# Optimization experiments

Measured on AMD Instinct MI355X. Metric: run time of the kernel, lower is better.

Reference implementation:

```python
import jax, jax.numpy as jnp
import numpy as np

D, H, G, HD = 2048, 16, 4, 128  # d_model, num_heads, num_groups, head_dim
B, S = 2, 2048


def _rope(x):
    # x: [B, heads, S, HD]; RoPE with concat(freqs, freqs) layout (rotate_half style)
    seq = x.shape[2]
    inv_freq = 1.0 / (10000.0 ** (jnp.arange(0, HD, 2, dtype=jnp.float32) / HD))  # [HD/2]
    t = jnp.arange(seq, dtype=jnp.float32)
    freqs = t[:, None] * inv_freq[None, :]              # [S, HD/2]
    emb = jnp.concatenate([freqs, freqs], axis=-1)      # [S, HD]
    cos = jnp.cos(emb)[None, None]                      # [1,1,S,HD]
    sin = jnp.sin(emb)[None, None]
    x1, x2 = jnp.split(x, 2, axis=-1)
    rot = jnp.concatenate([-x2, x1], axis=-1)           # rotate_half
    return x * cos + rot * sin


def setup_inputs() -> dict:
    key = jax.random.key(0)
    ks = jax.random.split(key, 5)
    x = jax.random.normal(ks[0], (B, S, D), dtype=jnp.float32)
    # weights stored as [in, out] so y = x @ W (equivalent to torch Linear with W^T)
    Wq = jax.random.normal(ks[1], (D, D), dtype=jnp.float32) * 0.02
    Wk = jax.random.normal(ks[2], (D, G * HD), dtype=jnp.float32) * 0.02
    Wv = jax.random.normal(ks[3], (D, G * HD), dtype=jnp.float32) * 0.02
    Wo = jax.random.normal(ks[4], (D, D), dtype=jnp.float32) * 0.02
    # causal mask: True = masked (matches torch masked_fill semantics)
    mask = ~jnp.tril(jnp.ones((S, S), dtype=bool))[None, None]  # [1,1,S,S]
    return {"x": x, "Wq": Wq, "Wk": Wk, "Wv": Wv, "Wo": Wo, "mask": mask}


def reference(x, Wq, Wk, Wv, Wo, mask):
    b, s, _ = x.shape
    q = (x @ Wq).reshape(b, s, H, HD).transpose(0, 2, 1, 3)   # [B,H,S,HD]
    k = (x @ Wk).reshape(b, s, G, HD).transpose(0, 2, 1, 3)   # [B,G,S,HD]
    v = (x @ Wv).reshape(b, s, G, HD).transpose(0, 2, 1, 3)   # [B,G,S,HD]
    q = _rope(q)
    k = _rope(k)
    # GQA: repeat_interleave KV groups across heads
    k = jnp.repeat(k, H // G, axis=1)                         # [B,H,S,HD]
    v = jnp.repeat(v, H // G, axis=1)
    scale = jnp.float32(1.0 / np.sqrt(HD))
    scores = jnp.einsum('bhqd,bhkd->bhqk', q, k) * scale      # [B,H,S,S]
    scores = jnp.where(mask, jnp.float32(-1e9), scores)
    attn = jax.nn.softmax(scores, axis=-1)
    ctx = jnp.einsum('bhqk,bhkd->bhqd', attn, v)              # [B,H,S,HD]
    ctx = ctx.transpose(0, 2, 1, 3).reshape(b, s, D)
    return ctx @ Wo
```

## Files before the change

### kernel.cpp

```cpp
#include <hip/hip_runtime.h>
#include <hip/hip_bf16.h>
#include <math.h>

#define BB 2
#define SS 2048
#define DD 2048
#define HH 16
#define GG 4
#define HDIM 128
#define DKV (GG * HDIM)
#define MS (BB * SS)
#define QKVS 3072

typedef __attribute__((ext_vector_type(8))) short bf16x8;
typedef __attribute__((ext_vector_type(4))) float f32x4;
typedef __attribute__((ext_vector_type(4))) unsigned int u32x4;

__device__ __forceinline__ ushort f2bf(float x) {
    __hip_bfloat16 b = __float2bfloat16(x);
    return *(ushort*)&b;
}
__device__ __forceinline__ float bf2f(ushort u) {
    __hip_bfloat16 b;
    *(ushort*)&b = u;
    return __bfloat162float(b);
}

#define GLOAD_LDS(src, dst)                                                        \
    __builtin_amdgcn_global_load_lds(                                              \
        (const __attribute__((address_space(1))) unsigned int*)(src),              \
        (__attribute__((address_space(3))) unsigned int*)(dst), 16, 0, 0)

#define WAITV(n) asm volatile("s_waitcnt vmcnt(" #n ")" ::: "memory")

__global__ void cast_bf16(const float* __restrict__ X, ushort* __restrict__ O, int total8) {
    int idx = blockIdx.x * blockDim.x + threadIdx.x;
    if (idx >= total8) return;
    const float4* p = (const float4*)X + (size_t)idx * 2;
    float4 a = p[0], b = p[1];
    float v[8] = {a.x, a.y, a.z, a.w, b.x, b.y, b.z, b.w};
    ushort r[8];
#pragma unroll
    for (int j = 0; j < 8; ++j) r[j] = f2bf(v[j]);
    *((u32x4*)O + idx) = *(u32x4*)r;
}

__global__ __launch_bounds__(256) void transpose_cast3(const float* __restrict__ Wq,
                                                       const float* __restrict__ Wk,
                                                       const float* __restrict__ Wv,
                                                       ushort* __restrict__ WqkvT) {
    __shared__ ushort tile[32][33];
    const int z = blockIdx.z;
    if (z > 0 && blockIdx.x >= DKV / 32) return;
    const float* W = (z == 0) ? Wq : (z == 1) ? Wk : Wv;
    ushort* WT = WqkvT + ((z == 0) ? (size_t)0 : (z == 1) ? (size_t)DD * DD
                                                          : (size_t)(DD + DKV) * DD);
    const int N = (z == 0) ? DD : DKV;
    const int tx = threadIdx.x & 31, ty = threadIdx.x >> 5;
    const int n0 = blockIdx.x * 32, k0 = blockIdx.y * 32;
#pragma unroll
    for (int i = 0; i < 4; ++i)
        tile[ty + i * 8][tx] = f2bf(W[(size_t)(k0 + ty + i * 8) * N + n0 + tx]);
    __syncthreads();
#pragma unroll
    for (int i = 0; i < 4; ++i)
        WT[(size_t)(n0 + ty + i * 8) * DD + k0 + tx] = tile[tx][ty + i * 8];
}

__global__ __launch_bounds__(256) void transpose_cast(const float* __restrict__ W,
                                                      ushort* __restrict__ WT,
                                                      int K, int N) {
    __shared__ ushort tile[32][33];
    const int tx = threadIdx.x & 31, ty = threadIdx.x >> 5;
    const int n0 = blockIdx.x * 32, k0 = blockIdx.y * 32;
#pragma unroll
    for (int i = 0; i < 4; ++i)
        tile[ty + i * 8][tx] = f2bf(W[(size_t)(k0 + ty + i * 8) * N + n0 + tx]);
    __syncthreads();
#pragma unroll
    for (int i = 0; i < 4; ++i)
        WT[(size_t)(n0 + ty + i * 8) * K + k0 + tx] = tile[tx][ty + i * 8];
}

__global__ __launch_bounds__(256) void transpose_v(const ushort* __restrict__ QKV,
                                                   ushort* __restrict__ VT) {
    __shared__ ushort tile[32][33];
    const int tx = threadIdx.x & 31, ty = threadIdx.x >> 5;
    const int d0 = blockIdx.x * 32;
    const int k0 = blockIdx.y * 32;
    const int b = blockIdx.z;
#pragma unroll
    for (int i = 0; i < 4; ++i)
        tile[ty + i * 8][tx] =
            QKV[(size_t)(b * SS + k0 + ty + i * 8) * QKVS + 2560 + d0 + tx];
    __syncthreads();
    const int posl = ((tx & 12) << 1) | ((tx & 16) >> 2) | (tx & 3);
#pragma unroll
    for (int i = 0; i < 4; ++i)
        VT[((size_t)b * DKV + d0 + ty + i * 8) * SS + k0 + posl] = tile[tx][ty + i * 8];
}

template <int BN, bool OUT_BF16>
__global__ __launch_bounds__(512) void gemm8(const ushort* __restrict__ A,
                                             const ushort* __restrict__ BT,
                                             void* __restrict__ Cout,
                                             int M, int N, int K) {
    constexpr int ABUF = 128 * 32;
    constexpr int BBUF = BN * 32;
    constexpr int NWC = BN / 64;
    constexpr int NWM = 8 / NWC;
    constexpr int ROWS = 128 / NWM;
    constexpr int MFR = ROWS / 16;
    __shared__ ushort As[3 * ABUF];
    __shared__ ushort Bs[3 * BBUF];

    const int t = threadIdx.x;
    const int w = t >> 6, l = t & 63;
    const int lm = l & 15, lw = l >> 4;
    const int wr = w / NWC, wc = w % NWC;
    const int nx = gridDim.x;
    const int bid = blockIdx.y * nx + blockIdx.x;
    const int cpx = (nx * gridDim.y) >> 3;
    const int swb = (bid & 7) * cpx + (bid >> 3);
    const int bm = (swb / nx) * 128, bn = (swb % nx) * BN;

    const int NT = K >> 5;
    const int swzc = (lw ^ ((lm >> 1) & 3)) * 8;

    const int ar0 = t >> 2, ac0 = (t & 3) ^ ((ar0 >> 1) & 3);
    const ushort* a0 = A + (size_t)(bm + ar0) * K + ac0 * 8;
    const int br0 = t >> 2, bc0 = (t & 3) ^ ((br0 >> 1) & 3);
    const ushort* b0 = BT + (size_t)(bn + br0) * K + bc0 * 8;
    const int br1 = (t + 512) >> 2, bc1 = ((t + 512) & 3) ^ ((br1 >> 1) & 3);
    const ushort* b1 = BT + (size_t)(bn + br1) * K + bc1 * 8;

    auto STAGE = [&](int slot) {
        GLOAD_LDS(a0, &As[slot * ABUF + t * 8]);
        a0 += 32;
        GLOAD_LDS(b0, &Bs[slot * BBUF + t * 8]);
        b0 += 32;
        if constexpr (BN == 256) {
            GLOAD_LDS(b1, &Bs[slot * BBUF + (t + 512) * 8]);
            b1 += 32;
        }
    };

    f32x4 acc[MFR][4];
#pragma unroll
    for (int m = 0; m < MFR; ++m)
#pragma unroll
        for (int n = 0; n < 4; ++n) acc[m][n] = (f32x4){0.f, 0.f, 0.f, 0.f};

    STAGE(0);
    STAGE(1);
    int cs = 0, ps = 2;

#pragma unroll 1
    for (int kt = 0; kt < NT; ++kt) {
        if (kt + 1 < NT) {
            if constexpr (BN == 256) WAITV(3); else WAITV(2);
        } else {
            WAITV(0);
        }
        __builtin_amdgcn_s_barrier();
        if (kt + 2 < NT) STAGE(ps);

        const ushort* Ab = &As[cs * ABUF];
        const ushort* Bb = &Bs[cs * BBUF];
        bf16x8 bfr[4], af[MFR];
#pragma unroll
        for (int n = 0; n < 4; ++n)
            bfr[n] = *(const bf16x8*)&Bb[(wc * 64 + n * 16 + lm) * 32 + swzc];
#pragma unroll
        for (int i = 0; i < MFR; ++i)
            af[i] = *(const bf16x8*)&Ab[(wr * ROWS + i * 16 + lm) * 32 + swzc];
        __builtin_amdgcn_s_setprio(1);
#pragma unroll
        for (int i = 0; i < MFR; ++i)
#pragma unroll
            for (int n = 0; n < 4; ++n)
                acc[i][n] = __builtin_amdgcn_mfma_f32_16x16x32_bf16(af[i], bfr[n], acc[i][n], 0, 0, 0);
        __builtin_amdgcn_s_setprio(0);

        cs = (cs == 2) ? 0 : cs + 1;
        ps = (ps == 2) ? 0 : ps + 1;
    }

#pragma unroll
    for (int m = 0; m < MFR; ++m)
#pragma unroll
        for (int n = 0; n < 4; ++n)
#pragma unroll
            for (int r = 0; r < 4; ++r) {
                int row = bm + wr * ROWS + m * 16 + lw * 4 + r;
                int col = bn + wc * 64 + n * 16 + lm;
                if (OUT_BF16)
                    ((ushort*)Cout)[(size_t)row * N + col] = f2bf(acc[m][n][r]);
                else
                    ((float*)Cout)[(size_t)row * N + col] = acc[m][n][r];
            }
}

__global__ void rope_bf16(ushort* __restrict__ X, int total) {
    int idx = blockIdx.x * blockDim.x + threadIdx.x;
    if (idx >= total) return;
    int i = idx & 63;
    int hh = (idx >> 6) % 20;
    int row = idx / (64 * 20);
    int s = row & (SS - 1);
    int colOff = (hh < 16) ? hh * HDIM : 2048 + (hh - 16) * HDIM;
    float inv = exp2f((float)i * -0.2076205059304601f);
    float ang = (float)s * inv;
    float c, sn;
    __sincosf(ang, &sn, &c);
    size_t base = (size_t)row * QKVS + colOff + i;
    float x1 = bf2f(X[base]), x2 = bf2f(X[base + 64]);
    X[base] = f2bf(x1 * c - x2 * sn);
    X[base + 64] = f2bf(x2 * c + x1 * sn);
}

#define SCL 0.08838834764831845f
#define CEXP 0.1275296340545927f
#define THRRAW 90.50966799187809f

__global__ __launch_bounds__(512) void attn_mfma(const ushort* __restrict__ QKV,
                                                 const ushort* __restrict__ VT,
                                                 ushort* __restrict__ Ctx) {
    __shared__ ushort Ks[3][64 * 128];
    __shared__ ushort Vs[3][128 * 64];
    const int t = threadIdx.x;
    const int w = t >> 6;
    const int l = t & 63;
    const int lm = l & 15, lw = l >> 4;
    const int bid = blockIdx.x;
    const int g = bid & 3;
    const int b = (bid >> 2) & 1;
    const int within = bid >> 3;
    const int xq = within & 7;
    const int h = g * 4 + (within >> 3);
    const int swz = (lm & 7) << 3;

    const ushort* kbase = QKV + (size_t)(b * SS) * QKVS + 2048 + g * HDIM;
    const ushort* vbase = VT + ((size_t)b * DKV + g * HDIM) * SS;

    const short one_bf = (short)0x3F80;
    const bf16x8 ones = {one_bf, one_bf, one_bf, one_bf, one_bf, one_bf, one_bf, one_bf};

    const int kr0 = t >> 4, ko0 = t & 15;
    const int kr1 = (t + 512) >> 4, ko1 = (t + 512) & 15;
    const int vr0 = t >> 3, vo0 = t & 7;
    const int vr1 = (t + 512) >> 3, vo1 = (t + 512) & 7;

#pragma unroll 1
    for (int phase = 0; phase < 2; ++phase) {
        const int qt = (phase == 0) ? xq : (15 - xq);
        const int q0 = qt * 128;
        const int qw = q0 + w * 16;
        const int q = qw + lm;
        const int ntiles = 2 * qt + 2;
        const int lt = (qw + 15) >> 6;

        const ushort* ks0 = kbase + (size_t)kr0 * QKVS + ((ko0 ^ (kr0 & 7)) * 8);
        const ushort* ks1 = kbase + (size_t)kr1 * QKVS + ((ko1 ^ (kr1 & 7)) * 8);
        const ushort* vs0 = vbase + (size_t)vr0 * SS + ((vo0 ^ (vr0 & 7)) * 8);
        const ushort* vs1 = vbase + (size_t)vr1 * SS + ((vo1 ^ (vr1 & 7)) * 8);

        auto STAGE = [&](int slot) {
            GLOAD_LDS(ks0, &Ks[slot][t * 8]);
            ks0 += 64 * QKVS;
            GLOAD_LDS(ks1, &Ks[slot][(t + 512) * 8]);
            ks1 += 64 * QKVS;
            GLOAD_LDS(vs0, &Vs[slot][t * 8]);
            vs0 += 64;
            GLOAD_LDS(vs1, &Vs[slot][(t + 512) * 8]);
            vs1 += 64;
        };

        bf16x8 qa[4];
        {
            const ushort* qp = QKV + (size_t)(b * SS + qw + lm) * QKVS + h * HDIM + lw * 8;
#pragma unroll
            for (int kk = 0; kk < 4; ++kk)
                qa[kk] = *(const bf16x8*)(qp + kk * 32);
        }

        f32x4 acc[8];
#pragma unroll
        for (int d = 0; d < 8; ++d) acc[d] = (f32x4){0.f, 0.f, 0.f, 0.f};
        f32x4 accl = (f32x4){0.f, 0.f, 0.f, 0.f};
        float m = -INFINITY;

        STAGE(0);
        STAGE(1);
        int cs = 0, ps = 2;

#pragma unroll 1
        for (int tile = 0; tile < ntiles; ++tile) {
            const int kv0 = tile * 64;
            if (tile + 1 < ntiles) {
                WAITV(4);
            } else {
                WAITV(0);
            }
            __builtin_amdgcn_s_barrier();
            if (tile + 2 < ntiles) STAGE(ps);

            if (tile <= lt) {
                f32x4 sfT[4];
#pragma unroll
                for (int kvb = 0; kvb < 4; ++kvb) sfT[kvb] = (f32x4){0.f, 0.f, 0.f, 0.f};
                __builtin_amdgcn_s_setprio(1);
#pragma unroll
                for (int kvb = 0; kvb < 4; ++kvb)
#pragma unroll
                    for (int kk = 0; kk < 4; ++kk) {
                        bf16x8 kb = *(const bf16x8*)&Ks[cs][(kvb * 16 + lm) * 128 + ((kk * 32 + lw * 8) ^ swz)];
                        sfT[kvb] = __builtin_amdgcn_mfma_f32_16x16x32_bf16(kb, qa[kk], sfT[kvb], 0, 0, 0);
                    }
                __builtin_amdgcn_s_setprio(0);

                if (tile == lt) {
#pragma unroll
                    for (int kvb = 0; kvb < 4; ++kvb)
#pragma unroll
                        for (int r = 0; r < 4; ++r) {
                            int kv = kv0 + kvb * 16 + lw * 4 + r;
                            if (kv > q) sfT[kvb][r] = -INFINITY;
                        }
                }

                float rm = fmaxf(fmaxf(sfT[0][0], sfT[0][1]), fmaxf(sfT[0][2], sfT[0][3]));
#pragma unroll
                for (int kvb = 1; kvb < 4; ++kvb)
                    rm = fmaxf(rm, fmaxf(fmaxf(sfT[kvb][0], sfT[kvb][1]),
                                         fmaxf(sfT[kvb][2], sfT[kvb][3])));
                rm = fmaxf(rm, __shfl_xor(rm, 16));
                rm = fmaxf(rm, __shfl_xor(rm, 32));

                bool stable = (rm - m <= THRRAW);
                if (!__all((int)stable)) {
                    float mn = fmaxf(m, rm);
                    float alpha_l = exp2f((m - mn) * CEXP);
                    m = mn;
                    float ar[4];
#pragma unroll
                    for (int r = 0; r < 4; ++r)
                        ar[r] = __shfl(alpha_l, (l & 48) | (lw * 4 + r));
#pragma unroll
                    for (int d = 0; d < 8; ++d) {
                        acc[d][0] *= ar[0];
                        acc[d][1] *= ar[1];
                        acc[d][2] *= ar[2];
                        acc[d][3] *= ar[3];
                    }
                    accl[0] *= ar[0];
                    accl[1] *= ar[1];
                    accl[2] *= ar[2];
                    accl[3] *= ar[3];
                }

                bf16x8 pa[2];
                float mC = m * CEXP;
#pragma unroll
                for (int kvb = 0; kvb < 4; ++kvb)
#pragma unroll
                    for (int r = 0; r < 4; ++r) {
                        float pv = exp2f(fmaf(sfT[kvb][r], CEXP, -mC));
                        pa[kvb >> 1][(kvb & 1) * 4 + r] = (short)f2bf(pv);
                    }

                __builtin_amdgcn_s_setprio(1);
#pragma unroll
                for (int kks = 0; kks < 2; ++kks) {
                    accl = __builtin_amdgcn_mfma_f32_16x16x32_bf16(pa[kks], ones, accl, 0, 0, 0);
#pragma unroll
                    for (int dcol = 0; dcol < 8; ++dcol) {
                        bf16x8 vb = *(const bf16x8*)&Vs[cs][(dcol * 16 + lm) * 64 + ((kks * 32 + lw * 8) ^ swz)];
                        acc[dcol] = __builtin_amdgcn_mfma_f32_16x16x32_bf16(pa[kks], vb, acc[dcol], 0, 0, 0);
                    }
                }
                __builtin_amdgcn_s_setprio(0);
            }

            cs = (cs == 2) ? 0 : cs + 1;
            ps = (ps == 2) ? 0 : ps + 1;
        }

        float rinv[4];
#pragma unroll
        for (int r = 0; r < 4; ++r) rinv[r] = 1.f / accl[r];
        ushort* cp = Ctx + (size_t)(b * SS + qw) * DD + h * HDIM;
#pragma unroll
        for (int d = 0; d < 8; ++d)
#pragma unroll
            for (int r = 0; r < 4; ++r)
                cp[(size_t)(lw * 4 + r) * DD + d * 16 + lm] = f2bf(acc[d][r] * rinv[r]);
        __builtin_amdgcn_s_barrier();
    }
}

extern "C" void kernel_launch(void* const* d_in, const int* in_sizes, int n_in,
                              void* d_out, int out_size, void* d_ws, size_t ws_size,
                              hipStream_t stream) {
    const float* x  = (const float*)d_in[0];
    const float* Wq = (const float*)d_in[1];
    const float* Wk = (const float*)d_in[2];
    const float* Wv = (const float*)d_in[3];
    const float* Wo = (const float*)d_in[4];
    float* out = (float*)d_out;

    ushort* xh    = (ushort*)d_ws;
    ushort* QKV   = xh + (size_t)MS * DD;
    ushort* VTb   = QKV + (size_t)MS * QKVS;
    ushort* WqkvT = VTb + (size_t)MS * DKV;
    ushort* WoT   = WqkvT + (size_t)QKVS * DD;
    ushort* Ch    = xh;

    dim3 blk(256);
    int nx8 = MS * DD / 8;
    cast_bf16<<<(nx8 + 255) / 256, 256, 0, stream>>>(x, xh, nx8);

    transpose_cast3<<<dim3(DD / 32, DD / 32, 3), blk, 0, stream>>>(Wq, Wk, Wv, WqkvT);

    gemm8<256, true><<<dim3(QKVS / 256, MS / 128), dim3(512), 0, stream>>>(xh, WqkvT, QKV, MS, QKVS, DD);

    int nrope = MS * 20 * 64;
    rope_bf16<<<(nrope + 255) / 256, 256, 0, stream>>>(QKV, nrope);

    transpose_v<<<dim3(DKV / 32, SS / 32, BB), blk, 0, stream>>>(QKV, VTb);

    attn_mfma<<<dim3(256), dim3(512), 0, stream>>>(QKV, VTb, Ch);

    transpose_cast<<<dim3(DD / 32, DD / 32), blk, 0, stream>>>(Wo, WoT, DD, DD);
    gemm8<128, false><<<dim3(DD / 128, MS / 128), dim3(512), 0, stream>>>(Ch, WoT, out, MS, DD, DD);
}
```

Before: 213.3 us.

## Software-pipeline attention loop so PV of previous tile overlaps current QK

Restructures the attention inner loop so the P·V matmul for tile t-1 is issued after the QK^T matmul for tile t, before the softmax of tile t. The aim is to hide the exp and max math behind MFMA work. K becomes double-buffered and V triple-buffered. Prefetch depth drops from two tiles to one, with a full vmcnt(0) wait and barrier at the end of each iteration. This may expose more global-load latency in exchange for better MFMA/VALU overlap, and it adds a tail PV step after the loop.

Result: no change. 213.3 us (+0.0%).

```diff
diff --git a/kernel.cpp b/kernel.cpp
--- a/kernel.cpp
+++ b/kernel.cpp
@@ -226,7 +226,7 @@
 __global__ __launch_bounds__(512) void attn_mfma(const ushort* __restrict__ QKV,
                                                  const ushort* __restrict__ VT,
                                                  ushort* __restrict__ Ctx) {
-    __shared__ ushort Ks[3][64 * 128];
+    __shared__ ushort Ks[2][64 * 128];
     __shared__ ushort Vs[3][128 * 64];
     const int t = threadIdx.x;
     const int w = t >> 6;
@@ -265,17 +265,6 @@
         const ushort* vs0 = vbase + (size_t)vr0 * SS + ((vo0 ^ (vr0 & 7)) * 8);
         const ushort* vs1 = vbase + (size_t)vr1 * SS + ((vo1 ^ (vr1 & 7)) * 8);
 
-        auto STAGE = [&](int slot) {
-            GLOAD_LDS(ks0, &Ks[slot][t * 8]);
-            ks0 += 64 * QKVS;
-            GLOAD_LDS(ks1, &Ks[slot][(t + 512) * 8]);
-            ks1 += 64 * QKVS;
-            GLOAD_LDS(vs0, &Vs[slot][t * 8]);
-            vs0 += 64;
-            GLOAD_LDS(vs1, &Vs[slot][(t + 512) * 8]);
-            vs1 += 64;
-        };
-
         bf16x8 qa[4];
         {
             const ushort* qp = QKV + (size_t)(b * SS + qw + lm) * QKVS + h * HDIM + lw * 8;
@@ -289,24 +278,55 @@
         for (int d = 0; d < 8; ++d) acc[d] = (f32x4){0.f, 0.f, 0.f, 0.f};
         f32x4 accl = (f32x4){0.f, 0.f, 0.f, 0.f};
         float m = -INFINITY;
-
-        STAGE(0);
-        STAGE(1);
-        int cs = 0, ps = 2;
+        bf16x8 pa[2] = {};
+
+        auto DO_PV = [&](int vslot) {
+            __builtin_amdgcn_s_setprio(1);
+#pragma unroll
+            for (int kks = 0; kks < 2; ++kks) {
+                accl = __builtin_amdgcn_mfma_f32_16x16x32_bf16(pa[kks], ones, accl, 0, 0, 0);
+#pragma unroll
+                for (int dcol = 0; dcol < 8; ++dcol) {
+                    bf16x8 vb = *(const bf16x8*)&Vs[vslot][(dcol * 16 + lm) * 64 + ((kks * 32 + lw * 8) ^ swz)];
+                    acc[dcol] = __builtin_amdgcn_mfma_f32_16x16x32_bf16(pa[kks], vb, acc[dcol], 0, 0, 0);
+                }
+            }
+            __builtin_amdgcn_s_setprio(0);
+        };
+
+        GLOAD_LDS(ks0, &Ks[0][t * 8]);
+        ks0 += 64 * QKVS;
+        GLOAD_LDS(ks1, &Ks[0][(t + 512) * 8]);
+        ks1 += 64 * QKVS;
+        GLOAD_LDS(vs0, &Vs[0][t * 8]);
+        vs0 += 64;
+        GLOAD_LDS(vs1, &Vs[0][(t + 512) * 8]);
+        vs1 += 64;
+        asm volatile("s_waitcnt vmcnt(0)" ::: "memory");
+        __builtin_amdgcn_s_barrier();
+
+        int vprev = 2, vcur = 0, vnext = 1;
 
 #pragma unroll 1
         for (int tile = 0; tile < ntiles; ++tile) {
             const int kv0 = tile * 64;
-            if (tile + 1 < ntiles) {
-                WAITV(4);
-            } else {
-                WAITV(0);
-            }
-            __builtin_amdgcn_s_barrier();
-            if (tile + 2 < ntiles) STAGE(ps);
-
-            if (tile <= lt) {
-                f32x4 sfT[4];
+            const bool more = (tile + 1 < ntiles);
+            if (more) {
+                ushort* kd = &Ks[(tile + 1) & 1][0];
+                ushort* vd = &Vs[vnext][0];
+                GLOAD_LDS(ks0, kd + t * 8);
+                ks0 += 64 * QKVS;
+                GLOAD_LDS(ks1, kd + (t + 512) * 8);
+                ks1 += 64 * QKVS;
+                GLOAD_LDS(vs0, vd + t * 8);
+                vs0 += 64;
+                GLOAD_LDS(vs1, vd + (t + 512) * 8);
+                vs1 += 64;
+            }
+
+            f32x4 sfT[4];
+            const bool active = (tile <= lt);
+            if (active) {
 #pragma unroll
                 for (int kvb = 0; kvb < 4; ++kvb) sfT[kvb] = (f32x4){0.f, 0.f, 0.f, 0.f};
                 __builtin_amdgcn_s_setprio(1);
@@ -314,11 +334,15 @@
                 for (int kvb = 0; kvb < 4; ++kvb)
 #pragma unroll
                     for (int kk = 0; kk < 4; ++kk) {
-                        bf16x8 kb = *(const bf16x8*)&Ks[cs][(kvb * 16 + lm) * 128 + ((kk * 32 + lw * 8) ^ swz)];
+                        bf16x8 kb = *(const bf16x8*)&Ks[tile & 1][(kvb * 16 + lm) * 128 + ((kk * 32 + lw * 8) ^ swz)];
                         sfT[kvb] = __builtin_amdgcn_mfma_f32_16x16x32_bf16(kb, qa[kk], sfT[kvb], 0, 0, 0);
                     }
                 __builtin_amdgcn_s_setprio(0);
-
+            }
+
+            if (tile >= 1 && tile <= lt + 1) DO_PV(vprev);
+
+            if (active) {
                 if (tile == lt) {
 #pragma unroll
                     for (int kvb = 0; kvb < 4; ++kvb)
@@ -328,7 +352,6 @@
                             if (kv > q) sfT[kvb][r] = -INFINITY;
                         }
                 }
-
                 float rm = fmaxf(fmaxf(sfT[0][0], sfT[0][1]), fmaxf(sfT[0][2], sfT[0][3]));
 #pragma unroll
                 for (int kvb = 1; kvb < 4; ++kvb)
@@ -359,7 +382,6 @@
                     accl[3] *= ar[3];
                 }
 
-                bf16x8 pa[2];
                 float mC = m * CEXP;
 #pragma unroll
                 for (int kvb = 0; kvb < 4; ++kvb)
@@ -368,23 +390,18 @@
                         float pv = exp2f(fmaf(sfT[kvb][r], CEXP, -mC));
                         pa[kvb >> 1][(kvb & 1) * 4 + r] = (short)f2bf(pv);
                     }
-
-                __builtin_amdgcn_s_setprio(1);
-#pragma unroll
-                for (int kks = 0; kks < 2; ++kks) {
-                    accl = __builtin_amdgcn_mfma_f32_16x16x32_bf16(pa[kks], ones, accl, 0, 0, 0);
-#pragma unroll
-                    for (int dcol = 0; dcol < 8; ++dcol) {
-                        bf16x8 vb = *(const bf16x8*)&Vs[cs][(dcol * 16 + lm) * 64 + ((kks * 32 + lw * 8) ^ swz)];
-                        acc[dcol] = __builtin_amdgcn_mfma_f32_16x16x32_bf16(pa[kks], vb, acc[dcol], 0, 0, 0);
-                    }
-                }
-                __builtin_amdgcn_s_setprio(0);
-            }
-
-            cs = (cs == 2) ? 0 : cs + 1;
-            ps = (ps == 2) ? 0 : ps + 1;
+            }
+
+            if (more) {
+                asm volatile("s_waitcnt vmcnt(0)" ::: "memory");
+                __builtin_amdgcn_s_barrier();
+            }
+            vprev = vcur;
+            vcur = vnext;
+            vnext = (vnext == 2) ? 0 : vnext + 1;
         }
+
+        if (lt == ntiles - 1) DO_PV(lt % 3);
 
         float rinv[4];
 #pragma unroll
```
